# Kernel optimization log

Hardware: AMD Instinct MI355X
Metric: run time of the kernel (lower is better)

## Reference

```python
import jax, jax.numpy as jnp
import numpy as np

N_HEADS = 16

def setup_inputs() -> dict:
    key = jax.random.key(0)
    k1, k2, k3, k4, k5 = jax.random.split(key, 5)
    B, T, C = 4, 2048, 1024
    x = jax.random.normal(k1, (B, T, C), dtype=jnp.float32)
    W_attn = jax.random.normal(k2, (C, 3 * C), dtype=jnp.float32) * 0.02
    b_attn = jnp.zeros((3 * C,), dtype=jnp.float32)
    W_proj = jax.random.normal(k3, (C, C), dtype=jnp.float32) * 0.02
    b_proj = jnp.zeros((C,), dtype=jnp.float32)
    return {"x": x, "W_attn": W_attn, "b_attn": b_attn, "W_proj": W_proj, "b_proj": b_proj}

def reference(x, W_attn, b_attn, W_proj, b_proj):
    B, T, C = x.shape
    H = N_HEADS
    hd = C // H
    qkv = x @ W_attn + b_attn                      # [B,T,3C]
    q, k, v = jnp.split(qkv, 3, axis=-1)
    q = q.reshape(B, T, H, hd)
    k = k.reshape(B, T, H, hd)
    v = v.reshape(B, T, H, hd)
    scale = 0.1 / jnp.sqrt(jnp.float32(hd))
    scores = jnp.einsum('bqhd,bkhd->bhqk', q, k) * scale   # [B,H,T,T]
    causal = jnp.tril(jnp.ones((T, T), dtype=bool))
    scores = jnp.where(causal[None, None], scores, jnp.float32(-jnp.inf))
    attn = jax.nn.softmax(scores, axis=-1)
    y = jnp.einsum('bhqk,bkhd->bqhd', attn, v).reshape(B, T, C)
    return y @ W_proj + b_proj
```

## Files before the change

### kernel.cpp

```cpp
#include <hip/hip_runtime.h>

typedef __attribute__((ext_vector_type(8))) __bf16 bf16x8;
typedef __attribute__((ext_vector_type(4))) float  f32x4;
typedef __attribute__((ext_vector_type(4))) short  short4v;
typedef __attribute__((ext_vector_type(4))) float  float4v;
typedef __attribute__((ext_vector_type(2))) unsigned int uint2v;

#define MFMA16(a,b,c) __builtin_amdgcn_mfma_f32_16x16x32_bf16((a),(b),(c),0,0,0)

__device__ __forceinline__ short f2bf(float f){
    unsigned int u = __builtin_bit_cast(unsigned int, f);
    u += 0x7fffu + ((u >> 16) & 1u);
    return (short)(u >> 16);
}

__device__ __forceinline__ unsigned int cvtpk(float a, float b){
    unsigned int w;
    asm("v_cvt_pk_bf16_f32 %0, %1, %2" : "=v"(w) : "v"(a), "v"(b));
    return w;
}

typedef __attribute__((address_space(1))) void gvoid;
typedef __attribute__((address_space(3))) void lvoid;
__device__ __forceinline__ void async_copy16(const void* g, void* l){
    __builtin_amdgcn_global_load_lds(
        (gvoid*)(unsigned long long)g,
        (lvoid*)(unsigned int)(unsigned long long)l,
        16, 0, 0);
}

#define BATCH 4
#define SEQ   2048
#define CDIM  1024
#define NH    16
#define HD    64
#define BT    8192
#define QSCALE 0.0125f
#define L2E 1.44269504088896340736f
#define DEFER_THR 8.0f

__global__ __launch_bounds__(256) void cvt_x(const float* __restrict__ x,
                                             short* __restrict__ xb){
    int idx = blockIdx.x * 256 + threadIdx.x;
    const float* s = x + (size_t)idx * 8;
    float4v a = *(const float4v*)(s);
    float4v b = *(const float4v*)(s + 4);
    short4v lo, hi;
#pragma unroll
    for (int j = 0; j < 4; ++j){ lo[j] = f2bf(a[j]); hi[j] = f2bf(b[j]); }
    short4v* d = (short4v*)(xb + (size_t)idx * 8);
    d[0] = lo; d[1] = hi;
}

__global__ __launch_bounds__(256) void wtrans(const float* __restrict__ W,
                                              short* __restrict__ Wt,
                                              int K, int N){
    __shared__ __align__(16) short lds[64 * 80];
    int tid = threadIdx.x;
    int n0 = blockIdx.x * 64, k0 = blockIdx.y * 64;
#pragma unroll
    for (int it = 0; it < 4; ++it){
        int idx = it * 256 + tid;
        int r = idx >> 4, c4 = (idx & 15) << 2;
        float4v w = *(const float4v*)(W + (size_t)(k0 + r) * N + n0 + c4);
        short4v h4;
#pragma unroll
        for (int j = 0; j < 4; ++j) h4[j] = f2bf(w[j]);
        *(short4v*)(&lds[r * 80 + c4]) = h4;
    }
    __syncthreads();
#pragma unroll
    for (int it = 0; it < 2; ++it){
        int idx = it * 256 + tid;
        int nl = idx >> 3, k8 = (idx & 7) << 3;
        short4v o0, o1;
#pragma unroll
        for (int j = 0; j < 4; ++j){
            o0[j] = lds[(k8 + j) * 80 + nl];
            o1[j] = lds[(k8 + 4 + j) * 80 + nl];
        }
        short4v* d = (short4v*)(Wt + (size_t)(n0 + nl) * K + k0 + k8);
        d[0] = o0; d[1] = o1;
    }
}

#define BM 128
#define BN 128
#define BK 32
#define KDIM 1024

__global__ __launch_bounds__(256) void qkv_gemm(const short* __restrict__ A,
                                                const short* __restrict__ Bt,
                                                const float* __restrict__ bias,
                                                short* __restrict__ q,
                                                short* __restrict__ k,
                                                short* __restrict__ v){
    __shared__ __align__(16) short As[2][BM * BK];
    __shared__ __align__(16) short Bs[2][BM * BK];
    const int tid = threadIdx.x;
    const int bn = blockIdx.x, bm = blockIdx.y;
    const int lane = tid & 63, wid = tid >> 6;
    const int wr = wid >> 1, wc = wid & 1;
    const int li = lane & 15, g = lane >> 4;
    const int arow0 = bm * BM, brow0 = bn * BN;

    f32x4 acc[4][4];
#pragma unroll
    for (int i = 0; i < 4; ++i)
#pragma unroll
        for (int j = 0; j < 4; ++j) acc[i][j] = f32x4{0.f,0.f,0.f,0.f};

    auto stage = [&](int buf, int kt){
        const short* ga = A  + (size_t)arow0 * KDIM + kt * BK;
        const short* gb = Bt + (size_t)brow0 * KDIM + kt * BK;
#pragma unroll
        for (int h = 0; h < 2; ++h){
            int f = h * 256 + tid;
            int row = f >> 2, kc = (f & 3) << 3;
            async_copy16(ga + (size_t)row * KDIM + kc, &As[buf][f << 3]);
            async_copy16(gb + (size_t)row * KDIM + kc, &Bs[buf][f << 3]);
        }
    };

    stage(0, 0);
    __syncthreads();
    int buf = 0;
    const int KT = KDIM / BK;
    for (int kt = 0; kt < KT; ++kt){
        if (kt + 1 < KT) stage(buf ^ 1, kt + 1);
        bf16x8 af[4], bfr[4];
#pragma unroll
        for (int mi = 0; mi < 4; ++mi)
            af[mi] = *(const bf16x8*)(&As[buf][(wr*64 + mi*16 + li) * BK + g*8]);
#pragma unroll
        for (int ni = 0; ni < 4; ++ni)
            bfr[ni] = *(const bf16x8*)(&Bs[buf][(wc*64 + ni*16 + li) * BK + g*8]);
#pragma unroll
        for (int mi = 0; mi < 4; ++mi)
#pragma unroll
            for (int ni = 0; ni < 4; ++ni)
                acc[mi][ni] = MFMA16(af[mi], bfr[ni], acc[mi][ni]);
        __syncthreads();
        buf ^= 1;
    }

    const int sec = bn >> 3;
    const int h   = ((bn & 7) << 1) | wc;
    short* dst = (sec == 0) ? q : ((sec == 1) ? k : v);
    const float mul = (sec == 0) ? QSCALE : 1.0f;
#pragma unroll
    for (int ni = 0; ni < 4; ++ni){
        int d = ni * 16 + li;
        float bb = bias[bn * 128 + wc * 64 + d];
#pragma unroll
        for (int mi = 0; mi < 4; ++mi){
#pragma unroll
            for (int r = 0; r < 4; ++r){
                int row = arow0 + wr * 64 + mi * 16 + g * 4 + r;
                int b_ = row >> 11, t = row & 2047;
                float val = (acc[mi][ni][r] + bb) * mul;
                dst[(((size_t)(b_ * NH + h)) * SEQ + t) * HD + d] = f2bf(val);
            }
        }
    }
}

__global__ __launch_bounds__(256) void proj_gemm(const short* __restrict__ A,
                                                 const short* __restrict__ Bt,
                                                 const float* __restrict__ bias,
                                                 float* __restrict__ out){
    __shared__ __align__(16) short As[2][BM * BK];
    __shared__ __align__(16) short Bs[2][BM * BK];
    const int tid = threadIdx.x;
    const int bn = blockIdx.x, bm = blockIdx.y;
    const int lane = tid & 63, wid = tid >> 6;
    const int wr = wid >> 1, wc = wid & 1;
    const int li = lane & 15, g = lane >> 4;
    const int arow0 = bm * BM, brow0 = bn * BN;

    f32x4 acc[4][4];
#pragma unroll
    for (int i = 0; i < 4; ++i)
#pragma unroll
        for (int j = 0; j < 4; ++j) acc[i][j] = f32x4{0.f,0.f,0.f,0.f};

    auto stage = [&](int buf, int kt){
        const short* ga = A  + (size_t)arow0 * KDIM + kt * BK;
        const short* gb = Bt + (size_t)brow0 * KDIM + kt * BK;
#pragma unroll
        for (int h = 0; h < 2; ++h){
            int f = h * 256 + tid;
            int row = f >> 2, kc = (f & 3) << 3;
            async_copy16(ga + (size_t)row * KDIM + kc, &As[buf][f << 3]);
            async_copy16(gb + (size_t)row * KDIM + kc, &Bs[buf][f << 3]);
        }
    };

    stage(0, 0);
    __syncthreads();
    int buf = 0;
    const int KT = KDIM / BK;
    for (int kt = 0; kt < KT; ++kt){
        if (kt + 1 < KT) stage(buf ^ 1, kt + 1);
        bf16x8 af[4], bfr[4];
#pragma unroll
        for (int mi = 0; mi < 4; ++mi)
            af[mi] = *(const bf16x8*)(&As[buf][(wr*64 + mi*16 + li) * BK + g*8]);
#pragma unroll
        for (int ni = 0; ni < 4; ++ni)
            bfr[ni] = *(const bf16x8*)(&Bs[buf][(wc*64 + ni*16 + li) * BK + g*8]);
#pragma unroll
        for (int mi = 0; mi < 4; ++mi)
#pragma unroll
            for (int ni = 0; ni < 4; ++ni)
                acc[mi][ni] = MFMA16(af[mi], bfr[ni], acc[mi][ni]);
        __syncthreads();
        buf ^= 1;
    }

#pragma unroll
    for (int ni = 0; ni < 4; ++ni){
        int c = brow0 + wc * 64 + ni * 16 + li;
        float bb = bias[c];
#pragma unroll
        for (int mi = 0; mi < 4; ++mi){
#pragma unroll
            for (int r = 0; r < 4; ++r){
                int row = arow0 + wr * 64 + mi * 16 + g * 4 + r;
                out[(size_t)row * CDIM + c] = acc[mi][ni][r] + bb;
            }
        }
    }
}

__global__ __launch_bounds__(256) void vtrans(const short* __restrict__ v,
                                              short* __restrict__ vt){
    __shared__ __align__(16) short lds[64 * 80];
    int tid = threadIdx.x;
    int t0 = blockIdx.x * 64;
    int bh = blockIdx.y;
    const short* src = v + ((size_t)bh * SEQ + t0) * HD;
#pragma unroll
    for (int it = 0; it < 2; ++it){
        int idx = it * 256 + tid;
        int r = idx >> 3, c8 = (idx & 7) << 3;
        *(bf16x8*)(&lds[r * 80 + c8]) = *(const bf16x8*)(src + (size_t)r * HD + c8);
    }
    __syncthreads();
    short* dst = vt + (size_t)bh * HD * SEQ + t0;
#pragma unroll
    for (int it = 0; it < 2; ++it){
        int idx = it * 256 + tid;
        int dl = idx >> 3, t8 = (idx & 7) << 3;
        short4v o0, o1;
#pragma unroll
        for (int j = 0; j < 4; ++j){
            o0[j] = lds[(t8 + j) * 80 + dl];
            o1[j] = lds[(t8 + 4 + j) * 80 + dl];
        }
        short4v* d = (short4v*)(dst + (size_t)dl * SEQ + t8);
        d[0] = o0; d[1] = o1;
    }
}

__global__ __launch_bounds__(256) void attn_kernel(const short* __restrict__ q,
                                                   const short* __restrict__ kk,
                                                   const short* __restrict__ vt,
                                                   short* __restrict__ y){
    __shared__ __align__(16) char kvs[2][2][8192];
    __shared__ __align__(16) char psm[4 * 2048];
    const int tid = threadIdx.x;
    const int qt = 31 - blockIdx.x;
    const int bh = blockIdx.y;
    const int lane = tid & 63, wid = tid >> 6;
    const int li = lane & 15, g = lane >> 4;
    const int iglob = qt * 64 + wid * 16 + li;

    const short* qp = q + ((size_t)bh * SEQ + iglob) * HD;
    bf16x8 qf0 = *(const bf16x8*)(qp + g * 8);
    bf16x8 qf1 = *(const bf16x8*)(qp + 32 + g * 8);

    char* pbase = psm + wid * 2048 + li * 128;
    const int sw = (li & 7) << 4;

    f32x4 acc[4];
#pragma unroll
    for (int df = 0; df < 4; ++df) acc[df] = f32x4{0.f,0.f,0.f,0.f};
    float m = -3e38f, l = 0.f;

    const short* kbp = kk + (size_t)bh * SEQ * HD;
    const short* vbp = vt + (size_t)bh * HD * SEQ;

    const int c0 = (wid * 2) * 64 + lane;
    const int r0 = c0 >> 3, sg0 = (c0 & 7) ^ (r0 & 7);
    const int c1 = c0 + 64;
    const int r1 = c1 >> 3, sg1 = (c1 & 7) ^ (r1 & 7);

    auto stage = [&](int b, int kt2){
        const int kb2 = kt2 * 64;
        const short* kg = kbp + (size_t)kb2 * HD;
        const short* vg = vbp + kb2;
        char* kd = kvs[b][0];
        char* vd = kvs[b][1];
        async_copy16(kg + r0 * HD + sg0 * 8, kd + c0 * 16);
        async_copy16(kg + r1 * HD + sg1 * 8, kd + c1 * 16);
        async_copy16(vg + (size_t)r0 * SEQ + sg0 * 8, vd + c0 * 16);
        async_copy16(vg + (size_t)r1 * SEQ + sg1 * 8, vd + c1 * 16);
    };

    stage(0, 0);
    asm volatile("s_waitcnt vmcnt(0)" ::: "memory");
    __builtin_amdgcn_s_barrier();
    int buf = 0;
    for (int kt = 0; kt <= qt; ++kt){
        const int kb = kt * 64;
        if (kt < qt) stage(buf ^ 1, kt + 1);

        const char* Kb = kvs[buf][0];
        const char* Vb = kvs[buf][1];

        f32x4 st[4];
#pragma unroll
        for (int kf = 0; kf < 4; ++kf) st[kf] = f32x4{0.f,0.f,0.f,0.f};
        __builtin_amdgcn_s_setprio(1);
#pragma unroll
        for (int kf = 0; kf < 4; ++kf){
            int r = kf * 16 + li;
            bf16x8 k0 = *(const bf16x8*)(Kb + r * 128 + ((g ^ (r & 7)) << 4));
            bf16x8 k1 = *(const bf16x8*)(Kb + r * 128 + (((g + 4) ^ (r & 7)) << 4));
            st[kf] = MFMA16(k0, qf0, st[kf]);
            st[kf] = MFMA16(k1, qf1, st[kf]);
        }
        __builtin_amdgcn_s_setprio(0);
        if (kt == qt){
#pragma unroll
            for (int kf = 0; kf < 4; ++kf)
#pragma unroll
                for (int r = 0; r < 4; ++r)
                    if (kb + kf * 16 + g * 4 + r > iglob) st[kf][r] = -3e38f;
        }
        float pm = -3e38f;
#pragma unroll
        for (int kf = 0; kf < 4; ++kf)
#pragma unroll
            for (int r = 0; r < 4; ++r) pm = fmaxf(pm, st[kf][r]);
        pm = fmaxf(pm, __shfl_xor(pm, 16, 64));
        pm = fmaxf(pm, __shfl_xor(pm, 32, 64));
        if (!__all(pm - m <= DEFER_THR)){
            float mnew = fmaxf(m, pm);
            float alpha = __builtin_amdgcn_exp2f((m - mnew) * L2E);
            l *= alpha;
#pragma unroll
            for (int df = 0; df < 4; ++df) acc[df] *= alpha;
            m = mnew;
        }
        const float nmL = -m * L2E;
        float rs = 0.f;
#pragma unroll
        for (int kf = 0; kf < 4; ++kf){
            float p0 = __builtin_amdgcn_exp2f(__builtin_fmaf(st[kf][0], L2E, nmL));
            float p1 = __builtin_amdgcn_exp2f(__builtin_fmaf(st[kf][1], L2E, nmL));
            float p2 = __builtin_amdgcn_exp2f(__builtin_fmaf(st[kf][2], L2E, nmL));
            float p3 = __builtin_amdgcn_exp2f(__builtin_fmaf(st[kf][3], L2E, nmL));
            rs += (p0 + p1) + (p2 + p3);
            uint2v pk = { cvtpk(p0, p1), cvtpk(p2, p3) };
            *(uint2v*)(pbase + (((kf << 5) + (g << 3)) ^ sw)) = pk;
        }
        rs += __shfl_xor(rs, 16, 64);
        rs += __shfl_xor(rs, 32, 64);
        l += rs;

        bf16x8 pb0 = *(const bf16x8*)(pbase + (((g << 4)) ^ sw));
        bf16x8 pb1 = *(const bf16x8*)(pbase + ((64 + (g << 4)) ^ sw));
        __builtin_amdgcn_s_setprio(1);
#pragma unroll
        for (int df = 0; df < 4; ++df){
            int d = df * 16 + li;
            bf16x8 v0 = *(const bf16x8*)(Vb + d * 128 + ((g ^ (d & 7)) << 4));
            bf16x8 v1 = *(const bf16x8*)(Vb + d * 128 + (((g + 4) ^ (d & 7)) << 4));
            acc[df] = MFMA16(v0, pb0, acc[df]);
            acc[df] = MFMA16(v1, pb1, acc[df]);
        }
        __builtin_amdgcn_s_setprio(0);

        asm volatile("s_waitcnt vmcnt(0)" ::: "memory");
        __builtin_amdgcn_s_barrier();
        buf ^= 1;
    }

    float rl = 1.f / l;
    const int b_ = bh >> 4, h = bh & 15;
    short* yp = y + ((size_t)(b_ * SEQ + iglob)) * CDIM + h * HD;
#pragma unroll
    for (int df = 0; df < 4; ++df){
        uint2v o = { cvtpk(acc[df][0] * rl, acc[df][1] * rl),
                     cvtpk(acc[df][2] * rl, acc[df][3] * rl) };
        *(uint2v*)(yp + df * 16 + g * 4) = o;
    }
}

extern "C" void kernel_launch(void* const* d_in, const int* in_sizes, int n_in,
                              void* d_out, int out_size, void* d_ws, size_t ws_size,
                              hipStream_t stream){
    const float* x      = (const float*)d_in[0];
    const float* W_attn = (const float*)d_in[1];
    const float* b_attn = (const float*)d_in[2];
    const float* W_proj = (const float*)d_in[3];
    const float* b_proj = (const float*)d_in[4];
    float* out = (float*)d_out;

    if (ws_size < (size_t)92274688) return;

    char* ws = (char*)d_ws;
    short* Wtp = (short*)(ws);
    short* q   = (short*)(ws + 2097152);
    short* kk  = (short*)(ws + 18874368);
    short* v   = (short*)(ws + 35651584);
    short* vt  = (short*)(ws + 52428800);
    short* xb  = (short*)(ws + 69206016);
    short* y   = xb;
    short* Wta = (short*)(ws + 85983232);

    cvt_x <<<4096, 256, 0, stream>>>(x, xb);
    wtrans<<<dim3(48, 16), 256, 0, stream>>>(W_attn, Wta, 1024, 3072);
    wtrans<<<dim3(16, 16), 256, 0, stream>>>(W_proj, Wtp, 1024, 1024);
    qkv_gemm<<<dim3(24, 64), 256, 0, stream>>>(xb, Wta, b_attn, q, kk, v);
    vtrans<<<dim3(32, 64), 256, 0, stream>>>(v, vt);
    attn_kernel<<<dim3(32, 64), 256, 0, stream>>>(q, kk, vt, y);
    proj_gemm<<<dim3(8, 64), 256, 0, stream>>>(y, Wtp, b_proj, out);
}
```

Baseline: 325.3 us.

## Process two query sub-tiles per wave to reuse each staged K/V tile

```diff
diff --git a/kernel.cpp b/kernel.cpp
--- a/kernel.cpp
+++ b/kernel.cpp
@@ -268,25 +268,33 @@
                                                    const short* __restrict__ vt,
                                                    short* __restrict__ y){
     __shared__ __align__(16) char kvs[2][2][8192];
-    __shared__ __align__(16) char psm[4 * 2048];
+    __shared__ __align__(16) char psm[4][2][2048];
     const int tid = threadIdx.x;
-    const int qt = 31 - blockIdx.x;
+    const int qt = 15 - blockIdx.x;
     const int bh = blockIdx.y;
     const int lane = tid & 63, wid = tid >> 6;
     const int li = lane & 15, g = lane >> 4;
-    const int iglob = qt * 64 + wid * 16 + li;
-
-    const short* qp = q + ((size_t)bh * SEQ + iglob) * HD;
-    bf16x8 qf0 = *(const bf16x8*)(qp + g * 8);
-    bf16x8 qf1 = *(const bf16x8*)(qp + 32 + g * 8);
-
-    char* pbase = psm + wid * 2048 + li * 128;
+    const int ig0 = qt * 128 + wid * 16 + li;
+    const int ig1 = ig0 + 64;
+
+    const short* qpA = q + ((size_t)bh * SEQ + ig0) * HD;
+    const short* qpB = q + ((size_t)bh * SEQ + ig1) * HD;
+    bf16x8 qA0 = *(const bf16x8*)(qpA + g * 8);
+    bf16x8 qA1 = *(const bf16x8*)(qpA + 32 + g * 8);
+    bf16x8 qB0 = *(const bf16x8*)(qpB + g * 8);
+    bf16x8 qB1 = *(const bf16x8*)(qpB + 32 + g * 8);
+
+    char* p0w = psm[wid][0] + li * 128;
+    char* p1w = psm[wid][1] + li * 128;
     const int sw = (li & 7) << 4;
 
-    f32x4 acc[4];
-#pragma unroll
-    for (int df = 0; df < 4; ++df) acc[df] = f32x4{0.f,0.f,0.f,0.f};
-    float m = -3e38f, l = 0.f;
+    f32x4 acc0[4], acc1[4];
+#pragma unroll
+    for (int df = 0; df < 4; ++df){
+        acc0[df] = f32x4{0.f,0.f,0.f,0.f};
+        acc1[df] = f32x4{0.f,0.f,0.f,0.f};
+    }
+    float m0 = -3e38f, l0 = 0.f, m1 = -3e38f, l1 = 0.f;
 
     const short* kbp = kk + (size_t)bh * SEQ * HD;
     const short* vbp = vt + (size_t)bh * HD * SEQ;
@@ -308,78 +316,110 @@
         async_copy16(vg + (size_t)r1 * SEQ + sg1 * 8, vd + c1 * 16);
     };
 
+    const int NT = 2 * qt + 2;
     stage(0, 0);
     asm volatile("s_waitcnt vmcnt(0)" ::: "memory");
     __builtin_amdgcn_s_barrier();
     int buf = 0;
-    for (int kt = 0; kt <= qt; ++kt){
+    for (int kt = 0; kt < NT; ++kt){
         const int kb = kt * 64;
-        if (kt < qt) stage(buf ^ 1, kt + 1);
+        if (kt + 1 < NT) stage(buf ^ 1, kt + 1);
 
         const char* Kb = kvs[buf][0];
         const char* Vb = kvs[buf][1];
 
-        f32x4 st[4];
-#pragma unroll
-        for (int kf = 0; kf < 4; ++kf) st[kf] = f32x4{0.f,0.f,0.f,0.f};
+        f32x4 st0[4], st1[4];
+#pragma unroll
+        for (int kf = 0; kf < 4; ++kf){
+            st0[kf] = f32x4{0.f,0.f,0.f,0.f};
+            st1[kf] = f32x4{0.f,0.f,0.f,0.f};
+        }
         __builtin_amdgcn_s_setprio(1);
 #pragma unroll
         for (int kf = 0; kf < 4; ++kf){
             int r = kf * 16 + li;
             bf16x8 k0 = *(const bf16x8*)(Kb + r * 128 + ((g ^ (r & 7)) << 4));
             bf16x8 k1 = *(const bf16x8*)(Kb + r * 128 + (((g + 4) ^ (r & 7)) << 4));
-            st[kf] = MFMA16(k0, qf0, st[kf]);
-            st[kf] = MFMA16(k1, qf1, st[kf]);
+            st0[kf] = MFMA16(k0, qA0, st0[kf]);
+            st0[kf] = MFMA16(k1, qA1, st0[kf]);
+            st1[kf] = MFMA16(k0, qB0, st1[kf]);
+            st1[kf] = MFMA16(k1, qB1, st1[kf]);
         }
         __builtin_amdgcn_s_setprio(0);
-        if (kt == qt){
+        if (kt >= 2 * qt){
 #pragma unroll
             for (int kf = 0; kf < 4; ++kf)
 #pragma unroll
                 for (int r = 0; r < 4; ++r)
-                    if (kb + kf * 16 + g * 4 + r > iglob) st[kf][r] = -3e38f;
-        }
-        float pm = -3e38f;
+                    if (kb + kf * 16 + g * 4 + r > ig0) st0[kf][r] = -3e38f;
+            if (kt == 2 * qt + 1){
+#pragma unroll
+                for (int kf = 0; kf < 4; ++kf)
+#pragma unroll
+                    for (int r = 0; r < 4; ++r)
+                        if (kb + kf * 16 + g * 4 + r > ig1) st1[kf][r] = -3e38f;
+            }
+        }
+        float pm0 = -3e38f, pm1 = -3e38f;
 #pragma unroll
         for (int kf = 0; kf < 4; ++kf)
 #pragma unroll
-            for (int r = 0; r < 4; ++r) pm = fmaxf(pm, st[kf][r]);
-        pm = fmaxf(pm, __shfl_xor(pm, 16, 64));
-        pm = fmaxf(pm, __shfl_xor(pm, 32, 64));
-        if (!__all(pm - m <= DEFER_THR)){
-            float mnew = fmaxf(m, pm);
-            float alpha = __builtin_amdgcn_exp2f((m - mnew) * L2E);
-            l *= alpha;
-#pragma unroll
-            for (int df = 0; df < 4; ++df) acc[df] *= alpha;
-            m = mnew;
-        }
-        const float nmL = -m * L2E;
-        float rs = 0.f;
+            for (int r = 0; r < 4; ++r){
+                pm0 = fmaxf(pm0, st0[kf][r]);
+                pm1 = fmaxf(pm1, st1[kf][r]);
+            }
+        pm0 = fmaxf(pm0, __shfl_xor(pm0, 16, 64));
+        pm0 = fmaxf(pm0, __shfl_xor(pm0, 32, 64));
+        pm1 = fmaxf(pm1, __shfl_xor(pm1, 16, 64));
+        pm1 = fmaxf(pm1, __shfl_xor(pm1, 32, 64));
+        if (!__all((pm0 - m0 <= DEFER_THR) && (pm1 - m1 <= DEFER_THR))){
+            float mn0 = fmaxf(m0, pm0), mn1 = fmaxf(m1, pm1);
+            float a0 = __builtin_amdgcn_exp2f((m0 - mn0) * L2E);
+            float a1 = __builtin_amdgcn_exp2f((m1 - mn1) * L2E);
+            l0 *= a0; l1 *= a1;
+#pragma unroll
+            for (int df = 0; df < 4; ++df){ acc0[df] *= a0; acc1[df] *= a1; }
+            m0 = mn0; m1 = mn1;
+        }
+        const float nm0 = -m0 * L2E, nm1 = -m1 * L2E;
+        float rs0 = 0.f, rs1 = 0.f;
 #pragma unroll
         for (int kf = 0; kf < 4; ++kf){
-            float p0 = __builtin_amdgcn_exp2f(__builtin_fmaf(st[kf][0], L2E, nmL));
-            float p1 = __builtin_amdgcn_exp2f(__builtin_fmaf(st[kf][1], L2E, nmL));
-            float p2 = __builtin_amdgcn_exp2f(__builtin_fmaf(st[kf][2], L2E, nmL));
-            float p3 = __builtin_amdgcn_exp2f(__builtin_fmaf(st[kf][3], L2E, nmL));
-            rs += (p0 + p1) + (p2 + p3);
-            uint2v pk = { cvtpk(p0, p1), cvtpk(p2, p3) };
-            *(uint2v*)(pbase + (((kf << 5) + (g << 3)) ^ sw)) = pk;
-        }
-        rs += __shfl_xor(rs, 16, 64);
-        rs += __shfl_xor(rs, 32, 64);
-        l += rs;
-
-        bf16x8 pb0 = *(const bf16x8*)(pbase + (((g << 4)) ^ sw));
-        bf16x8 pb1 = *(const bf16x8*)(pbase + ((64 + (g << 4)) ^ sw));
+            float a0 = __builtin_amdgcn_exp2f(__builtin_fmaf(st0[kf][0], L2E, nm0));
+            float a1 = __builtin_amdgcn_exp2f(__builtin_fmaf(st0[kf][1], L2E, nm0));
+            float a2 = __builtin_amdgcn_exp2f(__builtin_fmaf(st0[kf][2], L2E, nm0));
+            float a3 = __builtin_amdgcn_exp2f(__builtin_fmaf(st0[kf][3], L2E, nm0));
+            rs0 += (a0 + a1) + (a2 + a3);
+            uint2v pk0 = { cvtpk(a0, a1), cvtpk(a2, a3) };
+            *(uint2v*)(p0w + (((kf << 5) + (g << 3)) ^ sw)) = pk0;
+            float b0 = __builtin_amdgcn_exp2f(__builtin_fmaf(st1[kf][0], L2E, nm1));
+            float b1 = __builtin_amdgcn_exp2f(__builtin_fmaf(st1[kf][1], L2E, nm1));
+            float b2 = __builtin_amdgcn_exp2f(__builtin_fmaf(st1[kf][2], L2E, nm1));
+            float b3 = __builtin_amdgcn_exp2f(__builtin_fmaf(st1[kf][3], L2E, nm1));
+            rs1 += (b0 + b1) + (b2 + b3);
+            uint2v pk1 = { cvtpk(b0, b1), cvtpk(b2, b3) };
+            *(uint2v*)(p1w + (((kf << 5) + (g << 3)) ^ sw)) = pk1;
+        }
+        rs0 += __shfl_xor(rs0, 16, 64);
+        rs1 += __shfl_xor(rs1, 16, 64);
+        rs0 += __shfl_xor(rs0, 32, 64);
+        rs1 += __shfl_xor(rs1, 32, 64);
+        l0 += rs0; l1 += rs1;
+
+        bf16x8 p00 = *(const bf16x8*)(p0w + (((g << 4)) ^ sw));
+        bf16x8 p01 = *(const bf16x8*)(p0w + ((64 + (g << 4)) ^ sw));
+        bf16x8 p10 = *(const bf16x8*)(p1w + (((g << 4)) ^ sw));
+        bf16x8 p11 = *(const bf16x8*)(p1w + ((64 + (g << 4)) ^ sw));
         __builtin_amdgcn_s_setprio(1);
 #pragma unroll
         for (int df = 0; df < 4; ++df){
             int d = df * 16 + li;
             bf16x8 v0 = *(const bf16x8*)(Vb + d * 128 + ((g ^ (d & 7)) << 4));
             bf16x8 v1 = *(const bf16x8*)(Vb + d * 128 + (((g + 4) ^ (d & 7)) << 4));
-            acc[df] = MFMA16(v0, pb0, acc[df]);
-            acc[df] = MFMA16(v1, pb1, acc[df]);
+            acc0[df] = MFMA16(v0, p00, acc0[df]);
+            acc0[df] = MFMA16(v1, p01, acc0[df]);
+            acc1[df] = MFMA16(v0, p10, acc1[df]);
+            acc1[df] = MFMA16(v1, p11, acc1[df]);
         }
         __builtin_amdgcn_s_setprio(0);
 
@@ -388,14 +428,18 @@
         buf ^= 1;
     }
 
-    float rl = 1.f / l;
+    float rl0 = 1.f / l0, rl1 = 1.f / l1;
     const int b_ = bh >> 4, h = bh & 15;
-    short* yp = y + ((size_t)(b_ * SEQ + iglob)) * CDIM + h * HD;
+    short* yp0 = y + ((size_t)(b_ * SEQ + ig0)) * CDIM + h * HD;
+    short* yp1 = y + ((size_t)(b_ * SEQ + ig1)) * CDIM + h * HD;
 #pragma unroll
     for (int df = 0; df < 4; ++df){
-        uint2v o = { cvtpk(acc[df][0] * rl, acc[df][1] * rl),
-                     cvtpk(acc[df][2] * rl, acc[df][3] * rl) };
-        *(uint2v*)(yp + df * 16 + g * 4) = o;
+        uint2v o0 = { cvtpk(acc0[df][0] * rl0, acc0[df][1] * rl0),
+                      cvtpk(acc0[df][2] * rl0, acc0[df][3] * rl0) };
+        *(uint2v*)(yp0 + df * 16 + g * 4) = o0;
+        uint2v o1 = { cvtpk(acc1[df][0] * rl1, acc1[df][1] * rl1),
+                      cvtpk(acc1[df][2] * rl1, acc1[df][3] * rl1) };
+        *(uint2v*)(yp1 + df * 16 + g * 4) = o1;
     }
 }
 
@@ -426,6 +470,6 @@
     wtrans<<<dim3(16, 16), 256, 0, stream>>>(W_proj, Wtp, 1024, 1024);
     qkv_gemm<<<dim3(24, 64), 256, 0, stream>>>(xb, Wta, b_attn, q, kk, v);
     vtrans<<<dim3(32, 64), 256, 0, stream>>>(v, vt);
-    attn_kernel<<<dim3(32, 64), 256, 0, stream>>>(q, kk, vt, y);
+    attn_kernel<<<dim3(16, 64), 256, 0, stream>>>(q, kk, vt, y);
     proj_gemm<<<dim3(8, 64), 256, 0, stream>>>(y, Wtp, b_proj, out);
 }
```

After: 317.6 us. 1.02x faster.

## Enlarge attention query tile to 128 rows with 8 waves per block

Applied to the files above, without the earlier changes.

```diff
diff --git a/kernel.cpp b/kernel.cpp
--- a/kernel.cpp
+++ b/kernel.cpp
@@ -263,24 +263,24 @@
     }
 }
 
-__global__ __launch_bounds__(256) void attn_kernel(const short* __restrict__ q,
+__global__ __launch_bounds__(512) void attn_kernel(const short* __restrict__ q,
                                                    const short* __restrict__ kk,
                                                    const short* __restrict__ vt,
                                                    short* __restrict__ y){
     __shared__ __align__(16) char kvs[2][2][8192];
-    __shared__ __align__(16) char psm[4 * 2048];
+    __shared__ __align__(16) char psm[8][2048];
     const int tid = threadIdx.x;
-    const int qt = 31 - blockIdx.x;
+    const int qt = 15 - blockIdx.x;
     const int bh = blockIdx.y;
     const int lane = tid & 63, wid = tid >> 6;
     const int li = lane & 15, g = lane >> 4;
-    const int iglob = qt * 64 + wid * 16 + li;
-
-    const short* qp = q + ((size_t)bh * SEQ + iglob) * HD;
+    const int ig = qt * 128 + wid * 16 + li;
+
+    const short* qp = q + ((size_t)bh * SEQ + ig) * HD;
     bf16x8 qf0 = *(const bf16x8*)(qp + g * 8);
     bf16x8 qf1 = *(const bf16x8*)(qp + 32 + g * 8);
 
-    char* pbase = psm + wid * 2048 + li * 128;
+    char* pbase = psm[wid] + li * 128;
     const int sw = (li & 7) << 4;
 
     f32x4 acc[4];
@@ -291,30 +291,23 @@
     const short* kbp = kk + (size_t)bh * SEQ * HD;
     const short* vbp = vt + (size_t)bh * HD * SEQ;
 
-    const int c0 = (wid * 2) * 64 + lane;
+    const int c0 = wid * 64 + lane;
     const int r0 = c0 >> 3, sg0 = (c0 & 7) ^ (r0 & 7);
-    const int c1 = c0 + 64;
-    const int r1 = c1 >> 3, sg1 = (c1 & 7) ^ (r1 & 7);
 
     auto stage = [&](int b, int kt2){
         const int kb2 = kt2 * 64;
-        const short* kg = kbp + (size_t)kb2 * HD;
-        const short* vg = vbp + kb2;
-        char* kd = kvs[b][0];
-        char* vd = kvs[b][1];
-        async_copy16(kg + r0 * HD + sg0 * 8, kd + c0 * 16);
-        async_copy16(kg + r1 * HD + sg1 * 8, kd + c1 * 16);
-        async_copy16(vg + (size_t)r0 * SEQ + sg0 * 8, vd + c0 * 16);
-        async_copy16(vg + (size_t)r1 * SEQ + sg1 * 8, vd + c1 * 16);
+        async_copy16(kbp + ((size_t)(kb2 + r0)) * HD + sg0 * 8, kvs[b][0] + c0 * 16);
+        async_copy16(vbp + (size_t)r0 * SEQ + kb2 + sg0 * 8,    kvs[b][1] + c0 * 16);
     };
 
+    const int NT = 2 * qt + 2;
     stage(0, 0);
     asm volatile("s_waitcnt vmcnt(0)" ::: "memory");
     __builtin_amdgcn_s_barrier();
     int buf = 0;
-    for (int kt = 0; kt <= qt; ++kt){
+    for (int kt = 0; kt < NT; ++kt){
         const int kb = kt * 64;
-        if (kt < qt) stage(buf ^ 1, kt + 1);
+        if (kt + 1 < NT) stage(buf ^ 1, kt + 1);
 
         const char* Kb = kvs[buf][0];
         const char* Vb = kvs[buf][1];
@@ -332,12 +325,12 @@
             st[kf] = MFMA16(k1, qf1, st[kf]);
         }
         __builtin_amdgcn_s_setprio(0);
-        if (kt == qt){
+        if (kt >= 2 * qt){
 #pragma unroll
             for (int kf = 0; kf < 4; ++kf)
 #pragma unroll
                 for (int r = 0; r < 4; ++r)
-                    if (kb + kf * 16 + g * 4 + r > iglob) st[kf][r] = -3e38f;
+                    if (kb + kf * 16 + g * 4 + r > ig) st[kf][r] = -3e38f;
         }
         float pm = -3e38f;
 #pragma unroll
@@ -390,7 +383,7 @@
 
     float rl = 1.f / l;
     const int b_ = bh >> 4, h = bh & 15;
-    short* yp = y + ((size_t)(b_ * SEQ + iglob)) * CDIM + h * HD;
+    short* yp = y + ((size_t)(b_ * SEQ + ig)) * CDIM + h * HD;
 #pragma unroll
     for (int df = 0; df < 4; ++df){
         uint2v o = { cvtpk(acc[df][0] * rl, acc[df][1] * rl),
@@ -426,6 +419,6 @@
     wtrans<<<dim3(16, 16), 256, 0, stream>>>(W_proj, Wtp, 1024, 1024);
     qkv_gemm<<<dim3(24, 64), 256, 0, stream>>>(xb, Wta, b_attn, q, kk, v);
     vtrans<<<dim3(32, 64), 256, 0, stream>>>(v, vt);
-    attn_kernel<<<dim3(32, 64), 256, 0, stream>>>(q, kk, vt, y);
+    attn_kernel<<<dim3(16, 64), 512, 0, stream>>>(q, kk, vt, y);
     proj_gemm<<<dim3(8, 64), 256, 0, stream>>>(y, Wtp, b_proj, out);
 }
```

After: 308.2 us. -5.3%, faster.
